# Kernel tuning notes

Hardware: AMD Instinct MI355X
Metric: run time of the kernel (lower is better)

The kernel has to match this reference:

```python
import jax, jax.numpy as jnp
import numpy as np

ATT_DIM = 512
HEADS = 8
HEAD_DIM = ATT_DIM // HEADS
D_IN = 512
LEFT_MASK = 256
RIGHT_MASK = 0
LARGE = 1e30


def pos_encoding(S, d):
    # Transformer-XL sinusoid table over relative positions S-1 .. -(S-1), length 2S-1.
    inv_freq = (1.0 / (10000.0 ** (np.arange(0, d, 2.0) / d))).astype(np.float32)
    pos = jnp.arange(S - 1, -S, -1, dtype=jnp.float32)          # [2S-1]
    ang = pos[:, None] * jnp.asarray(inv_freq)[None, :]          # [2S-1, d/2]
    # concat([sin, cos], -1) on a trailing singleton -> interleaved sin/cos per frequency
    return jnp.stack([jnp.sin(ang), jnp.cos(ang)], axis=-1).reshape(2 * S - 1, d)


def rel_shift(x):
    # x: [B, N, S, 2S-1] -> [B, N, S, S] with out[i, j] = x[i, S-1 - i + j]
    B, N, S, L = x.shape
    x = jnp.pad(x, ((0, 0), (0, 0), (0, 0), (1, 0)))             # [B,N,S,L+1]
    x = x.reshape(B, N, L + 1, S)[:, :, 1:, :]                   # [B,N,L,S]
    x = x.reshape(B, N, S, L)
    return x[:, :, :, :S]


def setup_inputs() -> dict:
    key = jax.random.key(0)
    ks = jax.random.split(key, 9)
    B, S, D = 2, 2048, D_IN
    scale = 0.02
    return {
        "x": jax.random.normal(ks[0], (B, S, D), dtype=jnp.float32),
        "Wq": jax.random.normal(ks[1], (D, ATT_DIM), dtype=jnp.float32) * scale,
        "b_con": jax.random.normal(ks[2], (ATT_DIM,), dtype=jnp.float32) * scale,
        "b_rel": jax.random.normal(ks[3], (ATT_DIM,), dtype=jnp.float32) * scale,
        "Wk": jax.random.normal(ks[4], (D, ATT_DIM), dtype=jnp.float32) * scale,
        "Wkr": jax.random.normal(ks[5], (D_IN, ATT_DIM), dtype=jnp.float32) * scale,
        "Wv": jax.random.normal(ks[6], (D, ATT_DIM), dtype=jnp.float32) * scale,
        "bv": jax.random.normal(ks[7], (ATT_DIM,), dtype=jnp.float32) * scale,
        "x_len": jax.random.randint(ks[8], (B,), 1, S + 1).astype(jnp.int32),
    }


def reference(x, Wq, b_con, b_rel, Wk, Wkr, Wv, bv, x_len):
    B, S, D = x.shape
    N, Dh = HEADS, HEAD_DIM

    # content/relative query share the kernel (TiedDense) with separate biases
    q_lin = jnp.einsum('bsd,de->bse', x, Wq)
    q_con = (q_lin + b_con).reshape(B, S, N, Dh)
    q_rel = (q_lin + b_rel).reshape(B, S, N, Dh)
    k_con = jnp.einsum('bsd,de->bse', x, Wk).reshape(B, S, N, Dh)

    content_energy = jnp.einsum('bind,bjnd->bnij', q_con, k_con)  # [B,N,S,S]

    pos_emb = pos_encoding(S, D_IN)                               # [2S-1, D]
    k_rel = (pos_emb @ Wkr).reshape(2 * S - 1, N, Dh)
    relative_energy = jnp.einsum('bind,jnd->bnij', q_rel, k_rel)  # [B,N,S,2S-1]
    relative_energy = rel_shift(relative_energy)                  # [B,N,S,S]

    energy = (content_energy + relative_energy) / jnp.sqrt(jnp.float32(Dh))

    # sequence mask over keys (broadcast [B,1,1,S]) * banded mask (band_part)
    j = jnp.arange(S)
    seq_mask = (j[None, :] < x_len[:, None]).astype(jnp.float32)[:, None, None, :]
    i = jnp.arange(S)[:, None]
    band = ((i - j[None, :] <= LEFT_MASK) & (j[None, :] - i <= RIGHT_MASK)).astype(jnp.float32)
    mask = seq_mask * band[None, None, :, :]

    masked_energy = energy - (1.0 - mask) * LARGE
    attention = jax.nn.softmax(masked_energy, axis=-1)

    v = (jnp.einsum('bsd,de->bse', x, Wv) + bv).reshape(B, S, N, Dh)
    context = jnp.einsum('bnij,bjnd->bind', attention, v).reshape(B, S, N * Dh)
    return context
```

## Files before the change

### kernel.cpp

```cpp
#include <hip/hip_runtime.h>
#include <math.h>

#define S_ 2048
#define NH 8
#define DH 64
#define CSL 320
#define LP 72

typedef __attribute__((ext_vector_type(8))) short short8;
typedef __attribute__((ext_vector_type(4))) float f32x4;
typedef unsigned short ushort_t;

__device__ __forceinline__ short bf16r(float x) {
    union { float f; unsigned u; } v; v.f = x;
    unsigned r = v.u + 0x7fffu + ((v.u >> 16) & 1u);
    return (short)(r >> 16);
}
__device__ __forceinline__ float b2f(ushort_t h) {
    union { float f; unsigned u; } v; v.u = ((unsigned)h) << 16; return v.f;
}

__global__ __launch_bounds__(256) void prep_kernel(
    const float* __restrict__ x,
    const float* __restrict__ Wq, const float* __restrict__ Wk,
    const float* __restrict__ Wv, const float* __restrict__ Wkr,
    ushort_t* __restrict__ WTq, ushort_t* __restrict__ WTk,
    ushort_t* __restrict__ WTv, ushort_t* __restrict__ WTkr,
    ushort_t* __restrict__ pos, ushort_t* __restrict__ xb16)
{
    const int widx = blockIdx.z;
    const int t = threadIdx.x;
    if (widx == 4) {
        const int base = blockIdx.y * 8 + blockIdx.x;
        const float C = -0.051905126482615036f;
        const int f = t;
#pragma unroll
        for (int rep = 0; rep < 6; ++rep) {
            const int r = base + rep * 64;
            unsigned pk = 0;
            if (r <= 256) {
                float ang = (float)r * exp2f(C * (float)f);
                unsigned s = (unsigned)(ushort_t)bf16r(sinf(ang));
                unsigned c = (unsigned)(ushort_t)bf16r(cosf(ang));
                pk = s | (c << 16);
            }
            ((unsigned*)pos)[(size_t)r * 256 + f] = pk;
        }
        return;
    }
    if (widx == 5) {
        const int sub = blockIdx.y * 8 + blockIdx.x;
        const size_t base = (size_t)sub * 32768;
#pragma unroll
        for (int it = 0; it < 8; ++it) {
            const size_t idx = base + (size_t)it * 4096 + (size_t)t * 16;
            const float* src = &x[idx];
            ushort_t t16[16];
#pragma unroll
            for (int u = 0; u < 16; ++u) t16[u] = (ushort_t)bf16r(src[u]);
            *(short8*)&xb16[idx]     = *(short8*)&t16[0];
            *(short8*)&xb16[idx + 8] = *(short8*)&t16[8];
        }
        return;
    }
    const float* W = (widx == 0) ? Wq : (widx == 1) ? Wk : (widx == 2) ? Wv : Wkr;
    ushort_t* WT   = (widx == 0) ? WTq : (widx == 1) ? WTk : (widx == 2) ? WTv : WTkr;
    const int k0 = blockIdx.x * 64, n0 = blockIdx.y * 64;
    __shared__ __align__(16) ushort_t T[64][72];
    const int srow = t >> 2, sc0 = (t & 3) * 16;
    const float* src = &W[(size_t)(k0 + srow) * 512 + n0 + sc0];
#pragma unroll
    for (int u = 0; u < 16; ++u) T[sc0 + u][srow] = (ushort_t)bf16r(src[u]);
    __syncthreads();
    ushort_t* dst = &WT[(size_t)(n0 + srow) * 512 + k0 + sc0];
    *(short8*)dst       = *(const short8*)&T[srow][sc0];
    *(short8*)(dst + 8) = *(const short8*)&T[srow][sc0 + 8];
}

__global__ __launch_bounds__(256) void qkv_gemm(
    const ushort_t* __restrict__ xb16,
    const ushort_t* __restrict__ WTq, const ushort_t* __restrict__ WTk,
    const ushort_t* __restrict__ WTv,
    const ushort_t* __restrict__ pos, const ushort_t* __restrict__ WTkr,
    const float* __restrict__ b_con, const float* __restrict__ b_rel,
    const float* __restrict__ bv, const int* __restrict__ xlen_p,
    ushort_t* __restrict__ qcon, ushort_t* __restrict__ qrel,
    ushort_t* __restrict__ kout, ushort_t* __restrict__ vT,
    ushort_t* __restrict__ krel)
{
    const int widx = blockIdx.y >> 3;
    const int tid = threadIdx.x, lane = tid & 63, w = tid >> 6;
    const int quad = lane >> 4, l16 = lane & 15;

    __shared__ __align__(16) ushort_t A_lds[128][40];
    __shared__ __align__(16) ushort_t B_lds[64][40];

    f32x4 acc[2][4];
#pragma unroll
    for (int mt = 0; mt < 2; ++mt)
#pragma unroll
        for (int nt = 0; nt < 4; ++nt) acc[mt][nt] = (f32x4){0.f, 0.f, 0.f, 0.f};

    const int arow = tid >> 1, ak0 = (tid & 1) * 16;
    const int brow = tid >> 2, bk0 = (tid & 3) * 8;

    if (widx < 2) {
        const int m0 = blockIdx.x * 128;
        {
            const int xl = xlen_p[m0 >> 11];
            const int s0 = m0 & 2047;
            if (widx == 0) { if (s0 >= xl + 256) return; }
            else           { if (s0 >= xl + 63)  return; }
        }
        const int n0 = (blockIdx.y & 7) * 64;
        const ushort_t* WT = (widx == 0) ? WTq : WTk;
        const ushort_t* xrow = &xb16[(size_t)(m0 + arow) * 512 + ak0];
        const ushort_t* wrow = &WT[(size_t)(n0 + brow) * 512 + bk0];

        short8 pa0 = *(const short8*)xrow;
        short8 pa1 = *(const short8*)(xrow + 8);
        short8 pb  = *(const short8*)wrow;

#pragma unroll 1
        for (int k0 = 0; k0 < 512; k0 += 32) {
            __syncthreads();
            *(short8*)&A_lds[arow][ak0]     = pa0;
            *(short8*)&A_lds[arow][ak0 + 8] = pa1;
            *(short8*)&B_lds[brow][bk0]     = pb;
            if (k0 < 480) {
                pa0 = *(const short8*)(xrow + k0 + 32);
                pa1 = *(const short8*)(xrow + k0 + 40);
                pb  = *(const short8*)(wrow + k0 + 32);
            }
            __syncthreads();
            short8 a0 = *(const short8*)&A_lds[w * 32 + l16][quad * 8];
            short8 a1 = *(const short8*)&A_lds[w * 32 + 16 + l16][quad * 8];
#pragma unroll
            for (int nt = 0; nt < 4; ++nt) {
                short8 bb = *(const short8*)&B_lds[nt * 16 + l16][quad * 8];
                acc[0][nt] = __builtin_amdgcn_mfma_f32_16x16x32_bf16(a0, bb, acc[0][nt], 0, 0, 0);
                acc[1][nt] = __builtin_amdgcn_mfma_f32_16x16x32_bf16(a1, bb, acc[1][nt], 0, 0, 0);
            }
        }

#pragma unroll
        for (int nt = 0; nt < 4; ++nt) {
            const int col = n0 + nt * 16 + l16;
            float bc = 0.f, br = 0.f;
            if (widx == 0) { bc = b_con[col]; br = b_rel[col]; }
#pragma unroll
            for (int mt = 0; mt < 2; ++mt) {
#pragma unroll
                for (int reg = 0; reg < 4; ++reg) {
                    const size_t m = (size_t)(m0 + w * 32 + mt * 16 + quad * 4 + reg);
                    const float val = acc[mt][nt][reg];
                    if (widx == 0) {
                        qcon[m * 512 + col] = (ushort_t)bf16r((val + bc) * 0.125f);
                        qrel[m * 512 + col] = (ushort_t)bf16r((val + br) * 0.125f);
                    } else {
                        kout[m * 512 + col] = (ushort_t)bf16r(val);
                    }
                }
            }
        }
    } else if (widx == 2) {
        const int vb = (blockIdx.y & 7) * 32 + blockIdx.x;
        const int m0d = (vb & 3) * 128;
        const int n0j = (vb >> 2) * 64;
        const ushort_t* wrow = &WTv[(size_t)(m0d + arow) * 512 + ak0];
        const ushort_t* xrow = &xb16[(size_t)(n0j + brow) * 512 + bk0];

        short8 pa0 = *(const short8*)wrow;
        short8 pa1 = *(const short8*)(wrow + 8);
        short8 pb  = *(const short8*)xrow;

#pragma unroll 1
        for (int k0 = 0; k0 < 512; k0 += 32) {
            __syncthreads();
            *(short8*)&A_lds[arow][ak0]     = pa0;
            *(short8*)&A_lds[arow][ak0 + 8] = pa1;
            *(short8*)&B_lds[brow][bk0]     = pb;
            if (k0 < 480) {
                pa0 = *(const short8*)(wrow + k0 + 32);
                pa1 = *(const short8*)(wrow + k0 + 40);
                pb  = *(const short8*)(xrow + k0 + 32);
            }
            __syncthreads();
            short8 a0 = *(const short8*)&A_lds[w * 32 + l16][quad * 8];
            short8 a1 = *(const short8*)&A_lds[w * 32 + 16 + l16][quad * 8];
#pragma unroll
            for (int nt = 0; nt < 4; ++nt) {
                short8 bb = *(const short8*)&B_lds[nt * 16 + l16][quad * 8];
                acc[0][nt] = __builtin_amdgcn_mfma_f32_16x16x32_bf16(a0, bb, acc[0][nt], 0, 0, 0);
                acc[1][nt] = __builtin_amdgcn_mfma_f32_16x16x32_bf16(a1, bb, acc[1][nt], 0, 0, 0);
            }
        }

        const int b = n0j >> 11;
#pragma unroll
        for (int mt = 0; mt < 2; ++mt) {
#pragma unroll
            for (int reg = 0; reg < 4; ++reg) {
                const int d = m0d + w * 32 + mt * 16 + quad * 4 + reg;
                const int n = d >> 6, dd = d & 63;
                const float bvv = bv[d];
#pragma unroll
                for (int nt = 0; nt < 4; ++nt) {
                    const int s = (n0j + nt * 16 + l16) & 2047;
                    vT[((size_t)((b * NH + n) * 64 + dd)) * 2048 + s] =
                        (ushort_t)bf16r(acc[mt][nt][reg] + bvv);
                }
            }
        }
    } else {
        if (blockIdx.x >= 24) return;
        const int m0 = (blockIdx.x >> 3) * 128;
        const int n0 = (blockIdx.x & 7) * 64;
        const ushort_t* prow = &pos[(size_t)(m0 + arow) * 512 + ak0];
        const ushort_t* wrow = &WTkr[(size_t)(n0 + brow) * 512 + bk0];

        short8 pa0 = *(const short8*)prow;
        short8 pa1 = *(const short8*)(prow + 8);
        short8 pb  = *(const short8*)wrow;

#pragma unroll 1
        for (int k0 = 0; k0 < 512; k0 += 32) {
            __syncthreads();
            *(short8*)&A_lds[arow][ak0]     = pa0;
            *(short8*)&A_lds[arow][ak0 + 8] = pa1;
            *(short8*)&B_lds[brow][bk0]     = pb;
            if (k0 < 480) {
                pa0 = *(const short8*)(prow + k0 + 32);
                pa1 = *(const short8*)(prow + k0 + 40);
                pb  = *(const short8*)(wrow + k0 + 32);
            }
            __syncthreads();
            short8 a0 = *(const short8*)&A_lds[w * 32 + l16][quad * 8];
            short8 a1 = *(const short8*)&A_lds[w * 32 + 16 + l16][quad * 8];
#pragma unroll
            for (int nt = 0; nt < 4; ++nt) {
                short8 bb = *(const short8*)&B_lds[nt * 16 + l16][quad * 8];
                acc[0][nt] = __builtin_amdgcn_mfma_f32_16x16x32_bf16(a0, bb, acc[0][nt], 0, 0, 0);
                acc[1][nt] = __builtin_amdgcn_mfma_f32_16x16x32_bf16(a1, bb, acc[1][nt], 0, 0, 0);
            }
        }

#pragma unroll
        for (int nt = 0; nt < 4; ++nt) {
            const int col = n0 + nt * 16 + l16;
#pragma unroll
            for (int mt = 0; mt < 2; ++mt)
#pragma unroll
                for (int reg = 0; reg < 4; ++reg) {
                    const size_t m = (size_t)(m0 + w * 32 + mt * 16 + quad * 4 + reg);
                    krel[m * 512 + col] = (ushort_t)bf16r(acc[mt][nt][reg]);
                }
        }
    }
}

__global__ __launch_bounds__(256) void rel_gemm(
    const ushort_t* __restrict__ qrel, const ushort_t* __restrict__ krel,
    const ushort_t* __restrict__ vT, const int* __restrict__ xlen_p,
    ushort_t* __restrict__ R3, float* __restrict__ vmean)
{
    const int tile = blockIdx.x, n = blockIdx.y, b = blockIdx.z;
    const int tid = threadIdx.x, lane = tid & 63, w = tid >> 6;
    const int quad = lane >> 4, l16 = lane & 15;

    __shared__ __align__(16) ushort_t A_lds[128][LP];
    __shared__ __align__(16) ushort_t B_lds[64][LP];

    if (tile == 16) {
        const int row = tid >> 2, seg = tid & 3;
        const ushort_t* src = &vT[((size_t)((b * NH + n) * 64 + row)) * 2048 + seg * 512];
        float sum = 0.f;
        for (int it = 0; it < 64; ++it) {
            short8 h = *(const short8*)(src + it * 8);
#pragma unroll
            for (int u = 0; u < 8; ++u) sum += b2f((ushort_t)h[u]);
        }
        float* scratch = (float*)A_lds;
        scratch[row * 4 + seg] = sum;
        __syncthreads();
        if (tid < 64) {
            float s = scratch[tid * 4] + scratch[tid * 4 + 1]
                    + scratch[tid * 4 + 2] + scratch[tid * 4 + 3];
            vmean[(size_t)b * 512 + n * 64 + tid] = s * (1.0f / (float)S_);
        }
        return;
    }

    const int i0 = tile * 128;
    if (i0 >= xlen_p[b] + 256) return;

    {
        const int srow = tid >> 1, sc0 = (tid & 1) * 32;
        const ushort_t* src = &qrel[((size_t)b * S_ + i0 + srow) * 512 + n * 64 + sc0];
#pragma unroll
        for (int u = 0; u < 4; ++u)
            *(short8*)&A_lds[srow][sc0 + u * 8] = *(const short8*)(src + u * 8);
    }

    const size_t rbase3 = (size_t)(b * NH + n) * S_ * CSL;
    const int srow2 = tid >> 2, sc2 = (tid & 3) * 16;

    short8 pb0, pb1;
    auto issueB = [&](int rc) {
        const ushort_t* src = &krel[(size_t)(rc * 64 + srow2) * 512 + n * 64 + sc2];
        pb0 = *(const short8*)src;
        pb1 = *(const short8*)(src + 8);
    };
    issueB(0);

#pragma unroll 1
    for (int rc = 0; rc < 5; ++rc) {
        __syncthreads();
        *(short8*)&B_lds[srow2][sc2]     = pb0;
        *(short8*)&B_lds[srow2][sc2 + 8] = pb1;
        if (rc < 4) issueB(rc + 1);
        __syncthreads();

        short8 a[2][2];
#pragma unroll
        for (int mt = 0; mt < 2; ++mt) {
            a[mt][0] = *(const short8*)&A_lds[w * 32 + mt * 16 + l16][quad * 8];
            a[mt][1] = *(const short8*)&A_lds[w * 32 + mt * 16 + l16][quad * 8 + 32];
        }
#pragma unroll
        for (int nt = 0; nt < 4; ++nt) {
            short8 b0 = *(const short8*)&B_lds[nt * 16 + l16][quad * 8];
            short8 b1 = *(const short8*)&B_lds[nt * 16 + l16][quad * 8 + 32];
            const int r = rc * 64 + nt * 16 + l16;
#pragma unroll
            for (int mt = 0; mt < 2; ++mt) {
                f32x4 s = (f32x4){0.f, 0.f, 0.f, 0.f};
                s = __builtin_amdgcn_mfma_f32_16x16x32_bf16(a[mt][0], b0, s, 0, 0, 0);
                s = __builtin_amdgcn_mfma_f32_16x16x32_bf16(a[mt][1], b1, s, 0, 0, 0);
                if (r <= 256) {
#pragma unroll
                    for (int reg = 0; reg < 4; ++reg) {
                        const int ig = i0 + w * 32 + mt * 16 + quad * 4 + reg;
                        const int cslot = (ig & 31) + 256 - r;
                        R3[rbase3 + (size_t)ig * CSL + cslot] = (ushort_t)bf16r(s[reg]);
                    }
                }
            }
        }
    }
}

__global__ __launch_bounds__(128) void attn_kernel(
    const ushort_t* __restrict__ qcon, const ushort_t* __restrict__ kbuf,
    const ushort_t* __restrict__ vT, const ushort_t* __restrict__ R3,
    const float* __restrict__ vmean, const int* __restrict__ xlen_p,
    float* __restrict__ out)
{
    const int bx = blockIdx.x;
    const int tile = ((bx & 7) << 3) | (bx >> 3);
    const int n = blockIdx.y, b = blockIdx.z;
    const int i0 = tile * 32;
    const int tid = threadIdx.x, lane = tid & 63, w = tid >> 6;
    const int quad = lane >> 4, l16 = lane & 15;
    const int xlen = xlen_p[b];

    if (i0 >= xlen + 256) {
        const int row = tid >> 2, c0 = (tid & 3) * 16;
        const float* vm = &vmean[(size_t)b * 512 + n * 64 + c0];
        float* dst = &out[((size_t)b * S_ + i0 + row) * 512 + n * 64 + c0];
#pragma unroll
        for (int u = 0; u < 16; u += 4)
            *(float4*)&dst[u] = *(const float4*)&vm[u];
        return;
    }
    int nchunk = (xlen - i0 + 256 + 63) >> 6;
    if (nchunk > 5) nchunk = 5;

    __shared__ __align__(16) ushort_t q_lds[32][LP];
    __shared__ __align__(16) ushort_t k_lds[64][LP];
    __shared__ __align__(16) ushort_t vT_lds[64][LP];
    __shared__ __align__(16) ushort_t p_lds[32][LP];
    __shared__ __align__(16) ushort_t Rl_lds[32][LP];

    {
        const int qr = tid >> 2, qc = (tid & 3) * 16;
        const ushort_t* src = &qcon[((size_t)b * S_ + i0 + qr) * 512 + n * 64 + qc];
        *(short8*)&q_lds[qr][qc]     = *(const short8*)src;
        *(short8*)&q_lds[qr][qc + 8] = *(const short8*)(src + 8);
    }

    f32x4 Oa[4];
#pragma unroll
    for (int nt = 0; nt < 4; ++nt) Oa[nt] = (f32x4){0.f, 0.f, 0.f, 0.f};
    float lpart[4] = {};

    const size_t rbase3 = (size_t)(b * NH + n) * S_ * CSL;
    const size_t vTbase = (size_t)((b * NH + n) * 64) * 2048;
    const int srow = tid >> 1, sc0 = (tid & 1) * 32;
    const int rrow = tid >> 2, rcol = (tid & 3) * 16;
    const short8 z8 = {0, 0, 0, 0, 0, 0, 0, 0};

    short8 kr[4], vr[4], kn[4], vn[4];
    short8 rcur[2], rnxt[2];

    auto issue = [&](int c, short8* kd, short8* vd, short8* rd) {
        const int jc0 = i0 - 256 + c * 64;
        const int jg = jc0 + srow;
        const bool okk = (jg >= 0);
        const ushort_t* ks = &kbuf[((size_t)b * S_ + jg) * 512 + n * 64 + sc0];
        const ushort_t* vs = &vT[vTbase + (size_t)srow * 2048 + jc0 + sc0];
#pragma unroll
        for (int u = 0; u < 4; ++u) {
            kd[u] = okk ? *(const short8*)(ks + u * 8) : z8;
            const bool okv = (jc0 + sc0 + u * 8) >= 0;
            vd[u] = okv ? *(const short8*)(vs + u * 8) : z8;
        }
        const ushort_t* Rs = &R3[rbase3 + (size_t)(i0 + rrow) * CSL + c * 64 + rcol];
        rd[0] = *(const short8*)Rs;
        rd[1] = *(const short8*)(Rs + 8);
    };

    issue(0, kr, vr, rcur);

#pragma unroll 1
    for (int c = 0; c < nchunk; ++c) {
        const int jc0 = i0 - 256 + c * 64;
        __syncthreads();
#pragma unroll
        for (int u = 0; u < 4; ++u) {
            *(short8*)&k_lds[srow][sc0 + u * 8]  = kr[u];
            *(short8*)&vT_lds[srow][sc0 + u * 8] = vr[u];
        }
        *(short8*)&Rl_lds[rrow][rcol]     = rcur[0];
        *(short8*)&Rl_lds[rrow][rcol + 8] = rcur[1];
        if (c + 1 < nchunk) issue(c + 1, kn, vn, rnxt);
        __syncthreads();

        short8 aq0 = *(const short8*)&q_lds[w * 16 + l16][quad * 8];
        short8 aq1 = *(const short8*)&q_lds[w * 16 + l16][quad * 8 + 32];
        f32x4 Sacc[4];
#pragma unroll
        for (int jt = 0; jt < 4; ++jt) {
            short8 bk0 = *(const short8*)&k_lds[jt * 16 + l16][quad * 8];
            short8 bk1 = *(const short8*)&k_lds[jt * 16 + l16][quad * 8 + 32];
            f32x4 s = (f32x4){0.f, 0.f, 0.f, 0.f};
            s = __builtin_amdgcn_mfma_f32_16x16x32_bf16(aq0, bk0, s, 0, 0, 0);
            s = __builtin_amdgcn_mfma_f32_16x16x32_bf16(aq1, bk1, s, 0, 0, 0);
            Sacc[jt] = s;
        }

#pragma unroll
        for (int jt = 0; jt < 4; ++jt) {
#pragma unroll
            for (int reg = 0; reg < 4; ++reg) {
                const int row = w * 16 + quad * 4 + reg;
                const int i = i0 + row;
                const int j = jc0 + jt * 16 + l16;
                const int r = i - j;
                const bool valid = (j >= 0) && (j < xlen) && (r >= 0) && (r <= 256);
                float rvv = b2f(Rl_lds[row][jt * 16 + l16]);
                float e = valid ? __expf(Sacc[jt][reg] + rvv) : 0.f;
                lpart[reg] += e;
                p_lds[row][jt * 16 + l16] = (ushort_t)bf16r(e);
            }
        }
        __syncthreads();

        short8 ap0 = *(const short8*)&p_lds[w * 16 + l16][quad * 8];
        short8 ap1 = *(const short8*)&p_lds[w * 16 + l16][quad * 8 + 32];
#pragma unroll
        for (int nt = 0; nt < 4; ++nt) {
            short8 bv0 = *(const short8*)&vT_lds[nt * 16 + l16][quad * 8];
            short8 bv1 = *(const short8*)&vT_lds[nt * 16 + l16][quad * 8 + 32];
            Oa[nt] = __builtin_amdgcn_mfma_f32_16x16x32_bf16(ap0, bv0, Oa[nt], 0, 0, 0);
            Oa[nt] = __builtin_amdgcn_mfma_f32_16x16x32_bf16(ap1, bv1, Oa[nt], 0, 0, 0);
        }

#pragma unroll
        for (int u = 0; u < 4; ++u) { kr[u] = kn[u]; vr[u] = vn[u]; }
        rcur[0] = rnxt[0]; rcur[1] = rnxt[1];
    }

#pragma unroll
    for (int reg = 0; reg < 4; ++reg) {
#pragma unroll
        for (int off = 1; off < 16; off <<= 1)
            lpart[reg] += __shfl_xor(lpart[reg], off, 64);
    }

#pragma unroll
    for (int reg = 0; reg < 4; ++reg) {
        const int i = i0 + w * 16 + quad * 4 + reg;
        const bool dead = (i >= xlen + 256);
        const float linv = 1.0f / lpart[reg];
#pragma unroll
        for (int nt = 0; nt < 4; ++nt) {
            const int d = n * 64 + nt * 16 + l16;
            float val = dead ? vmean[(size_t)b * 512 + d] : Oa[nt][reg] * linv;
            out[((size_t)b * S_ + i) * 512 + d] = val;
        }
    }
}

extern "C" void kernel_launch(void* const* d_in, const int* in_sizes, int n_in,
                              void* d_out, int out_size, void* d_ws, size_t ws_size,
                              hipStream_t stream) {
    const float* x     = (const float*)d_in[0];
    const float* Wq    = (const float*)d_in[1];
    const float* b_con = (const float*)d_in[2];
    const float* b_rel = (const float*)d_in[3];
    const float* Wk    = (const float*)d_in[4];
    const float* Wkr   = (const float*)d_in[5];
    const float* Wv    = (const float*)d_in[6];
    const float* bv    = (const float*)d_in[7];
    const int*   xlen  = (const int*)d_in[8];
    float* out = (float*)d_out;

    float* ws = (float*)d_ws;
    float* vmean = ws;
    ushort_t* ub   = (ushort_t*)(vmean + 1024);
    ushort_t* R3   = ub;
    ushort_t* qcon = R3   + 10485760;
    ushort_t* kbuf = qcon + 2097152;
    ushort_t* vT   = kbuf + 2097152;
    ushort_t* qrel = vT   + 2097152;
    ushort_t* xb16 = qrel + 2097152;
    ushort_t* krel = xb16 + 2097152;
    ushort_t* pos  = krel + 196608;
    ushort_t* WTq  = pos  + 196608;
    ushort_t* WTk  = WTq + 262144;
    ushort_t* WTv  = WTk + 262144;
    ushort_t* WTkr = WTv + 262144;

    prep_kernel<<<dim3(8, 8, 6), 256, 0, stream>>>(x, Wq, Wk, Wv, Wkr,
                                                   WTq, WTk, WTv, WTkr, pos, xb16);
    qkv_gemm<<<dim3(32, 25), 256, 0, stream>>>(xb16, WTq, WTk, WTv, pos, WTkr,
                                               b_con, b_rel, bv, xlen,
                                               qcon, qrel, kbuf, vT, krel);
    rel_gemm<<<dim3(17, 8, 2), 256, 0, stream>>>(qrel, krel, vT, xlen, R3, vmean);
    attn_kernel<<<dim3(64, 8, 2), 128, 0, stream>>>(qcon, kbuf, vT, R3, vmean,
                                                    xlen, out);
}
```

Measured before the change: 131.1 us.

## Fuse relative-position GEMM into attention kernel and compute V mean algebraically

Removes the separate rel_gemm kernel and its large R3 global scratch buffer. Each attention block now computes its own relative-energy band with MFMA from qrel and krel directly into a widened LDS tile, and reuses that tile for the probabilities. The V mean used for fully masked rows is computed as mean(x)·Wv + bv, using column partial sums taken in the prep kernel and a small extra block row in qkv_gemm. This cuts one launch and a large global write/read, at the cost of more LDS per attention block and extra MFMA work inside the attention kernel.

```diff
diff --git a/kernel.cpp b/kernel.cpp
--- a/kernel.cpp
+++ b/kernel.cpp
@@ -3,9 +3,8 @@
 
 #define S_ 2048
 #define NH 8
-#define DH 64
-#define CSL 320
 #define LP 72
+#define RP 328
 
 typedef __attribute__((ext_vector_type(8))) short short8;
 typedef __attribute__((ext_vector_type(4))) float f32x4;
@@ -26,7 +25,8 @@
     const float* __restrict__ Wv, const float* __restrict__ Wkr,
     ushort_t* __restrict__ WTq, ushort_t* __restrict__ WTk,
     ushort_t* __restrict__ WTv, ushort_t* __restrict__ WTkr,
-    ushort_t* __restrict__ pos, ushort_t* __restrict__ xb16)
+    ushort_t* __restrict__ pos, ushort_t* __restrict__ xb16,
+    float* __restrict__ xpart)
 {
     const int widx = blockIdx.z;
     const int t = threadIdx.x;
@@ -63,6 +63,19 @@
         }
         return;
     }
+    if (widx == 6) {
+        const int sub = blockIdx.y * 8 + blockIdx.x;
+        const int b = sub >> 5, rb = sub & 31;
+        const float* src = &x[((size_t)b * 2048 + (size_t)rb * 64) * 512];
+        float s0 = 0.f, s1 = 0.f;
+        for (int r = 0; r < 64; ++r) {
+            s0 += src[(size_t)r * 512 + t];
+            s1 += src[(size_t)r * 512 + t + 256];
+        }
+        xpart[(size_t)sub * 512 + t]       = s0;
+        xpart[(size_t)sub * 512 + t + 256] = s1;
+        return;
+    }
     const float* W = (widx == 0) ? Wq : (widx == 1) ? Wk : (widx == 2) ? Wv : Wkr;
     ushort_t* WT   = (widx == 0) ? WTq : (widx == 1) ? WTk : (widx == 2) ? WTv : WTkr;
     const int k0 = blockIdx.x * 64, n0 = blockIdx.y * 64;
@@ -84,9 +97,10 @@
     const ushort_t* __restrict__ pos, const ushort_t* __restrict__ WTkr,
     const float* __restrict__ b_con, const float* __restrict__ b_rel,
     const float* __restrict__ bv, const int* __restrict__ xlen_p,
+    const float* __restrict__ xpart,
     ushort_t* __restrict__ qcon, ushort_t* __restrict__ qrel,
     ushort_t* __restrict__ kout, ushort_t* __restrict__ vT,
-    ushort_t* __restrict__ krel)
+    ushort_t* __restrict__ krel, float* __restrict__ vmean)
 {
     const int widx = blockIdx.y >> 3;
     const int tid = threadIdx.x, lane = tid & 63, w = tid >> 6;
@@ -213,6 +227,36 @@
             }
         }
     } else {
+        if (blockIdx.y == 25) {
+            if (blockIdx.x >= 8) return;
+            float* xm = (float*)A_lds;
+            for (int idx = tid; idx < 1024; idx += 256) {
+                const int bb = idx >> 9, k = idx & 511;
+                float s = 0.f;
+                for (int p = 0; p < 32; ++p)
+                    s += xpart[(size_t)(bb * 32 + p) * 512 + k];
+                xm[bb * 512 + k] = s * (1.0f / 2048.0f);
+            }
+            __syncthreads();
+            if (tid < 64) {
+                const int d = blockIdx.x * 64 + tid;
+                const ushort_t* wrow = &WTv[(size_t)d * 512];
+                float a0 = 0.f, a1 = 0.f;
+                for (int k = 0; k < 512; k += 8) {
+                    short8 wv = *(const short8*)(wrow + k);
+#pragma unroll
+                    for (int u = 0; u < 8; ++u) {
+                        const float wf = b2f((ushort_t)wv[u]);
+                        a0 += xm[k + u] * wf;
+                        a1 += xm[512 + k + u] * wf;
+                    }
+                }
+                const float bvd = bv[d];
+                vmean[d]       = a0 + bvd;
+                vmean[512 + d] = a1 + bvd;
+            }
+            return;
+        }
         if (blockIdx.x >= 24) return;
         const int m0 = (blockIdx.x >> 3) * 128;
         const int n0 = (blockIdx.x & 7) * 64;
@@ -259,102 +303,11 @@
     }
 }
 
-__global__ __launch_bounds__(256) void rel_gemm(
-    const ushort_t* __restrict__ qrel, const ushort_t* __restrict__ krel,
-    const ushort_t* __restrict__ vT, const int* __restrict__ xlen_p,
-    ushort_t* __restrict__ R3, float* __restrict__ vmean)
-{
-    const int tile = blockIdx.x, n = blockIdx.y, b = blockIdx.z;
-    const int tid = threadIdx.x, lane = tid & 63, w = tid >> 6;
-    const int quad = lane >> 4, l16 = lane & 15;
-
-    __shared__ __align__(16) ushort_t A_lds[128][LP];
-    __shared__ __align__(16) ushort_t B_lds[64][LP];
-
-    if (tile == 16) {
-        const int row = tid >> 2, seg = tid & 3;
-        const ushort_t* src = &vT[((size_t)((b * NH + n) * 64 + row)) * 2048 + seg * 512];
-        float sum = 0.f;
-        for (int it = 0; it < 64; ++it) {
-            short8 h = *(const short8*)(src + it * 8);
-#pragma unroll
-            for (int u = 0; u < 8; ++u) sum += b2f((ushort_t)h[u]);
-        }
-        float* scratch = (float*)A_lds;
-        scratch[row * 4 + seg] = sum;
-        __syncthreads();
-        if (tid < 64) {
-            float s = scratch[tid * 4] + scratch[tid * 4 + 1]
-                    + scratch[tid * 4 + 2] + scratch[tid * 4 + 3];
-            vmean[(size_t)b * 512 + n * 64 + tid] = s * (1.0f / (float)S_);
-        }
-        return;
-    }
-
-    const int i0 = tile * 128;
-    if (i0 >= xlen_p[b] + 256) return;
-
-    {
-        const int srow = tid >> 1, sc0 = (tid & 1) * 32;
-        const ushort_t* src = &qrel[((size_t)b * S_ + i0 + srow) * 512 + n * 64 + sc0];
-#pragma unroll
-        for (int u = 0; u < 4; ++u)
-            *(short8*)&A_lds[srow][sc0 + u * 8] = *(const short8*)(src + u * 8);
-    }
-
-    const size_t rbase3 = (size_t)(b * NH + n) * S_ * CSL;
-    const int srow2 = tid >> 2, sc2 = (tid & 3) * 16;
-
-    short8 pb0, pb1;
-    auto issueB = [&](int rc) {
-        const ushort_t* src = &krel[(size_t)(rc * 64 + srow2) * 512 + n * 64 + sc2];
-        pb0 = *(const short8*)src;
-        pb1 = *(const short8*)(src + 8);
-    };
-    issueB(0);
-
-#pragma unroll 1
-    for (int rc = 0; rc < 5; ++rc) {
-        __syncthreads();
-        *(short8*)&B_lds[srow2][sc2]     = pb0;
-        *(short8*)&B_lds[srow2][sc2 + 8] = pb1;
-        if (rc < 4) issueB(rc + 1);
-        __syncthreads();
-
-        short8 a[2][2];
-#pragma unroll
-        for (int mt = 0; mt < 2; ++mt) {
-            a[mt][0] = *(const short8*)&A_lds[w * 32 + mt * 16 + l16][quad * 8];
-            a[mt][1] = *(const short8*)&A_lds[w * 32 + mt * 16 + l16][quad * 8 + 32];
-        }
-#pragma unroll
-        for (int nt = 0; nt < 4; ++nt) {
-            short8 b0 = *(const short8*)&B_lds[nt * 16 + l16][quad * 8];
-            short8 b1 = *(const short8*)&B_lds[nt * 16 + l16][quad * 8 + 32];
-            const int r = rc * 64 + nt * 16 + l16;
-#pragma unroll
-            for (int mt = 0; mt < 2; ++mt) {
-                f32x4 s = (f32x4){0.f, 0.f, 0.f, 0.f};
-                s = __builtin_amdgcn_mfma_f32_16x16x32_bf16(a[mt][0], b0, s, 0, 0, 0);
-                s = __builtin_amdgcn_mfma_f32_16x16x32_bf16(a[mt][1], b1, s, 0, 0, 0);
-                if (r <= 256) {
-#pragma unroll
-                    for (int reg = 0; reg < 4; ++reg) {
-                        const int ig = i0 + w * 32 + mt * 16 + quad * 4 + reg;
-                        const int cslot = (ig & 31) + 256 - r;
-                        R3[rbase3 + (size_t)ig * CSL + cslot] = (ushort_t)bf16r(s[reg]);
-                    }
-                }
-            }
-        }
-    }
-}
-
 __global__ __launch_bounds__(128) void attn_kernel(
-    const ushort_t* __restrict__ qcon, const ushort_t* __restrict__ kbuf,
-    const ushort_t* __restrict__ vT, const ushort_t* __restrict__ R3,
-    const float* __restrict__ vmean, const int* __restrict__ xlen_p,
-    float* __restrict__ out)
+    const ushort_t* __restrict__ qcon, const ushort_t* __restrict__ qrel,
+    const ushort_t* __restrict__ kbuf, const ushort_t* __restrict__ vT,
+    const ushort_t* __restrict__ krel, const float* __restrict__ vmean,
+    const int* __restrict__ xlen_p, float* __restrict__ out)
 {
     const int bx = blockIdx.x;
     const int tile = ((bx & 7) << 3) | (bx >> 3);
@@ -365,9 +318,9 @@
     const int xlen = xlen_p[b];
 
     if (i0 >= xlen + 256) {
-        const int row = tid >> 2, c0 = (tid & 3) * 16;
-        const float* vm = &vmean[(size_t)b * 512 + n * 64 + c0];
-        float* dst = &out[((size_t)b * S_ + i0 + row) * 512 + n * 64 + c0];
+        const int row = tid >> 2, c0f = (tid & 3) * 16;
+        const float* vm = &vmean[(size_t)b * 512 + n * 64 + c0f];
+        float* dst = &out[((size_t)b * S_ + i0 + row) * 512 + n * 64 + c0f];
 #pragma unroll
         for (int u = 0; u < 16; u += 4)
             *(float4*)&dst[u] = *(const float4*)&vm[u];
@@ -375,18 +328,46 @@
     }
     int nchunk = (xlen - i0 + 256 + 63) >> 6;
     if (nchunk > 5) nchunk = 5;
-
-    __shared__ __align__(16) ushort_t q_lds[32][LP];
+    const int c0 = (i0 < 256) ? ((256 - i0) >> 6) : 0;
+
     __shared__ __align__(16) ushort_t k_lds[64][LP];
     __shared__ __align__(16) ushort_t vT_lds[64][LP];
-    __shared__ __align__(16) ushort_t p_lds[32][LP];
-    __shared__ __align__(16) ushort_t Rl_lds[32][LP];
+    __shared__ __align__(16) ushort_t R_lds[32][RP];
+
+    const ushort_t* qc = &qcon[((size_t)b * S_ + i0 + w * 16 + l16) * 512 + n * 64 + quad * 8];
+    const short8 aq0 = *(const short8*)qc;
+    const short8 aq1 = *(const short8*)(qc + 32);
 
     {
-        const int qr = tid >> 2, qc = (tid & 3) * 16;
-        const ushort_t* src = &qcon[((size_t)b * S_ + i0 + qr) * 512 + n * 64 + qc];
-        *(short8*)&q_lds[qr][qc]     = *(const short8*)src;
-        *(short8*)&q_lds[qr][qc + 8] = *(const short8*)(src + 8);
+        const ushort_t* qr = &qrel[((size_t)b * S_ + i0 + w * 16 + l16) * 512 + n * 64 + quad * 8];
+        const short8 ar0 = *(const short8*)qr;
+        const short8 ar1 = *(const short8*)(qr + 32);
+        const ushort_t* kb = &krel[(size_t)l16 * 512 + n * 64 + quad * 8];
+        int ntmin = w + 16 - 4 * nchunk; if (ntmin < 0) ntmin = 0;
+        const int ntmax = w + 17 - 4 * c0;
+        const ushort_t* pb = kb + (size_t)ntmin * 8192;
+        short8 br0 = *(const short8*)pb;
+        short8 br1 = *(const short8*)(pb + 32);
+#pragma unroll 1
+        for (int nt = ntmin; nt < ntmax; ++nt) {
+            short8 nb0, nb1;
+            if (nt + 1 < ntmax) {
+                const ushort_t* pn = kb + (size_t)(nt + 1) * 8192;
+                nb0 = *(const short8*)pn;
+                nb1 = *(const short8*)(pn + 32);
+            }
+            f32x4 acc = (f32x4){0.f, 0.f, 0.f, 0.f};
+            acc = __builtin_amdgcn_mfma_f32_16x16x32_bf16(ar0, br0, acc, 0, 0, 0);
+            acc = __builtin_amdgcn_mfma_f32_16x16x32_bf16(ar1, br1, acc, 0, 0, 0);
+            const int r = nt * 16 + l16;
+#pragma unroll
+            for (int reg = 0; reg < 4; ++reg) {
+                const int rowq = w * 16 + quad * 4 + reg;
+                const int cs = rowq + 256 - r;
+                if (cs >= 0) R_lds[rowq][cs] = (ushort_t)bf16r(acc[reg]);
+            }
+            br0 = nb0; br1 = nb1;
+        }
     }
 
     f32x4 Oa[4];
@@ -394,16 +375,13 @@
     for (int nt = 0; nt < 4; ++nt) Oa[nt] = (f32x4){0.f, 0.f, 0.f, 0.f};
     float lpart[4] = {};
 
-    const size_t rbase3 = (size_t)(b * NH + n) * S_ * CSL;
     const size_t vTbase = (size_t)((b * NH + n) * 64) * 2048;
     const int srow = tid >> 1, sc0 = (tid & 1) * 32;
-    const int rrow = tid >> 2, rcol = (tid & 3) * 16;
     const short8 z8 = {0, 0, 0, 0, 0, 0, 0, 0};
 
     short8 kr[4], vr[4], kn[4], vn[4];
-    short8 rcur[2], rnxt[2];
-
-    auto issue = [&](int c, short8* kd, short8* vd, short8* rd) {
+
+    auto issue = [&](int c, short8* kd, short8* vd) {
         const int jc0 = i0 - 256 + c * 64;
         const int jg = jc0 + srow;
         const bool okk = (jg >= 0);
@@ -415,15 +393,12 @@
             const bool okv = (jc0 + sc0 + u * 8) >= 0;
             vd[u] = okv ? *(const short8*)(vs + u * 8) : z8;
         }
-        const ushort_t* Rs = &R3[rbase3 + (size_t)(i0 + rrow) * CSL + c * 64 + rcol];
-        rd[0] = *(const short8*)Rs;
-        rd[1] = *(const short8*)(Rs + 8);
     };
 
-    issue(0, kr, vr, rcur);
+    issue(c0, kr, vr);
 
 #pragma unroll 1
-    for (int c = 0; c < nchunk; ++c) {
+    for (int c = c0; c < nchunk; ++c) {
         const int jc0 = i0 - 256 + c * 64;
         __syncthreads();
 #pragma unroll
@@ -431,13 +406,9 @@
             *(short8*)&k_lds[srow][sc0 + u * 8]  = kr[u];
             *(short8*)&vT_lds[srow][sc0 + u * 8] = vr[u];
         }
-        *(short8*)&Rl_lds[rrow][rcol]     = rcur[0];
-        *(short8*)&Rl_lds[rrow][rcol + 8] = rcur[1];
-        if (c + 1 < nchunk) issue(c + 1, kn, vn, rnxt);
+        if (c + 1 < nchunk) issue(c + 1, kn, vn);
         __syncthreads();
 
-        short8 aq0 = *(const short8*)&q_lds[w * 16 + l16][quad * 8];
-        short8 aq1 = *(const short8*)&q_lds[w * 16 + l16][quad * 8 + 32];
         f32x4 Sacc[4];
 #pragma unroll
         for (int jt = 0; jt < 4; ++jt) {
@@ -458,16 +429,16 @@
                 const int j = jc0 + jt * 16 + l16;
                 const int r = i - j;
                 const bool valid = (j >= 0) && (j < xlen) && (r >= 0) && (r <= 256);
-                float rvv = b2f(Rl_lds[row][jt * 16 + l16]);
+                float rvv = b2f(R_lds[row][c * 64 + jt * 16 + l16]);
                 float e = valid ? __expf(Sacc[jt][reg] + rvv) : 0.f;
                 lpart[reg] += e;
-                p_lds[row][jt * 16 + l16] = (ushort_t)bf16r(e);
+                R_lds[row][c * 64 + jt * 16 + l16] = (ushort_t)bf16r(e);
             }
         }
         __syncthreads();
 
-        short8 ap0 = *(const short8*)&p_lds[w * 16 + l16][quad * 8];
-        short8 ap1 = *(const short8*)&p_lds[w * 16 + l16][quad * 8 + 32];
+        short8 ap0 = *(const short8*)&R_lds[w * 16 + l16][c * 64 + quad * 8];
+        short8 ap1 = *(const short8*)&R_lds[w * 16 + l16][c * 64 + quad * 8 + 32];
 #pragma unroll
         for (int nt = 0; nt < 4; ++nt) {
             short8 bv0 = *(const short8*)&vT_lds[nt * 16 + l16][quad * 8];
@@ -478,7 +449,6 @@
 
 #pragma unroll
         for (int u = 0; u < 4; ++u) { kr[u] = kn[u]; vr[u] = vn[u]; }
-        rcur[0] = rnxt[0]; rcur[1] = rnxt[1];
     }
 
 #pragma unroll
@@ -519,8 +489,8 @@
     float* ws = (float*)d_ws;
     float* vmean = ws;
     ushort_t* ub   = (ushort_t*)(vmean + 1024);
-    ushort_t* R3   = ub;
-    ushort_t* qcon = R3   + 10485760;
+    float* xpart   = (float*)ub;
+    ushort_t* qcon = ub   + 10485760;
     ushort_t* kbuf = qcon + 2097152;
     ushort_t* vT   = kbuf + 2097152;
     ushort_t* qrel = vT   + 2097152;
@@ -532,12 +502,12 @@
     ushort_t* WTv  = WTk + 262144;
     ushort_t* WTkr = WTv + 262144;
 
-    prep_kernel<<<dim3(8, 8, 6), 256, 0, stream>>>(x, Wq, Wk, Wv, Wkr,
-                                                   WTq, WTk, WTv, WTkr, pos, xb16);
-    qkv_gemm<<<dim3(32, 25), 256, 0, stream>>>(xb16, WTq, WTk, WTv, pos, WTkr,
-                                               b_con, b_rel, bv, xlen,
-                                               qcon, qrel, kbuf, vT, krel);
-    rel_gemm<<<dim3(17, 8, 2), 256, 0, stream>>>(qrel, krel, vT, xlen, R3, vmean);
-    attn_kernel<<<dim3(64, 8, 2), 128, 0, stream>>>(qcon, kbuf, vT, R3, vmean,
-                                                    xlen, out);
+    prep_kernel<<<dim3(8, 8, 7), 256, 0, stream>>>(x, Wq, Wk, Wv, Wkr,
+                                                   WTq, WTk, WTv, WTkr, pos, xb16,
+                                                   xpart);
+    qkv_gemm<<<dim3(32, 26), 256, 0, stream>>>(xb16, WTq, WTk, WTv, pos, WTkr,
+                                               b_con, b_rel, bv, xlen, xpart,
+                                               qcon, qrel, kbuf, vT, krel, vmean);
+    attn_kernel<<<dim3(64, 8, 2), 128, 0, stream>>>(qcon, qrel, kbuf, vT, krel,
+                                                    vmean, xlen, out);
 }
```

Measured after the change: 136.5 us. 4.1% more time.

## Enlarge attention query tile to 64 rows and skip fully-negative key chunks

Applied to the files above, without the earlier changes.

The attention kernel now processes 64 query rows per block with 256 threads instead of 32 rows with 128, so each staged K/V chunk in shared memory is reused by twice as many queries. The R3 column-slot layout in rel_gemm changes to match the 64-row tile. Query fragments are loaded straight into registers instead of through LDS, and chunks lying entirely before position zero are skipped by starting the loop at c0, which removes the j>=0 guards. This halves the grid and raises per-block LDS use, which may lower occupancy.

```diff
diff --git a/kernel.cpp b/kernel.cpp
--- a/kernel.cpp
+++ b/kernel.cpp
@@ -3,7 +3,6 @@
 
 #define S_ 2048
 #define NH 8
-#define DH 64
 #define CSL 320
 #define LP 72
 
@@ -341,7 +340,7 @@
 #pragma unroll
                     for (int reg = 0; reg < 4; ++reg) {
                         const int ig = i0 + w * 32 + mt * 16 + quad * 4 + reg;
-                        const int cslot = (ig & 31) + 256 - r;
+                        const int cslot = (ig & 63) + 256 - r;
                         R3[rbase3 + (size_t)ig * CSL + cslot] = (ushort_t)bf16r(s[reg]);
                     }
                 }
@@ -350,24 +349,24 @@
     }
 }
 
-__global__ __launch_bounds__(128) void attn_kernel(
+__global__ __launch_bounds__(256) void attn_kernel(
     const ushort_t* __restrict__ qcon, const ushort_t* __restrict__ kbuf,
     const ushort_t* __restrict__ vT, const ushort_t* __restrict__ R3,
     const float* __restrict__ vmean, const int* __restrict__ xlen_p,
     float* __restrict__ out)
 {
     const int bx = blockIdx.x;
-    const int tile = ((bx & 7) << 3) | (bx >> 3);
+    const int tile = ((bx & 7) << 2) | (bx >> 3);
     const int n = blockIdx.y, b = blockIdx.z;
-    const int i0 = tile * 32;
+    const int i0 = tile * 64;
     const int tid = threadIdx.x, lane = tid & 63, w = tid >> 6;
     const int quad = lane >> 4, l16 = lane & 15;
     const int xlen = xlen_p[b];
 
     if (i0 >= xlen + 256) {
-        const int row = tid >> 2, c0 = (tid & 3) * 16;
-        const float* vm = &vmean[(size_t)b * 512 + n * 64 + c0];
-        float* dst = &out[((size_t)b * S_ + i0 + row) * 512 + n * 64 + c0];
+        const int row = tid >> 2, cf = (tid & 3) * 16;
+        const float* vm = &vmean[(size_t)b * 512 + n * 64 + cf];
+        float* dst = &out[((size_t)b * S_ + i0 + row) * 512 + n * 64 + cf];
 #pragma unroll
         for (int u = 0; u < 16; u += 4)
             *(float4*)&dst[u] = *(const float4*)&vm[u];
@@ -375,19 +374,16 @@
     }
     int nchunk = (xlen - i0 + 256 + 63) >> 6;
     if (nchunk > 5) nchunk = 5;
-
-    __shared__ __align__(16) ushort_t q_lds[32][LP];
+    const int c0 = (i0 < 256) ? ((256 - i0) >> 6) : 0;
+
     __shared__ __align__(16) ushort_t k_lds[64][LP];
     __shared__ __align__(16) ushort_t vT_lds[64][LP];
-    __shared__ __align__(16) ushort_t p_lds[32][LP];
-    __shared__ __align__(16) ushort_t Rl_lds[32][LP];
-
-    {
-        const int qr = tid >> 2, qc = (tid & 3) * 16;
-        const ushort_t* src = &qcon[((size_t)b * S_ + i0 + qr) * 512 + n * 64 + qc];
-        *(short8*)&q_lds[qr][qc]     = *(const short8*)src;
-        *(short8*)&q_lds[qr][qc + 8] = *(const short8*)(src + 8);
-    }
+    __shared__ __align__(16) ushort_t p_lds[64][LP];
+    __shared__ __align__(16) ushort_t Rl_lds[64][LP];
+
+    const ushort_t* qc = &qcon[((size_t)b * S_ + i0 + w * 16 + l16) * 512 + n * 64 + quad * 8];
+    const short8 aq0 = *(const short8*)qc;
+    const short8 aq1 = *(const short8*)(qc + 32);
 
     f32x4 Oa[4];
 #pragma unroll
@@ -396,48 +392,38 @@
 
     const size_t rbase3 = (size_t)(b * NH + n) * S_ * CSL;
     const size_t vTbase = (size_t)((b * NH + n) * 64) * 2048;
-    const int srow = tid >> 1, sc0 = (tid & 1) * 32;
-    const int rrow = tid >> 2, rcol = (tid & 3) * 16;
-    const short8 z8 = {0, 0, 0, 0, 0, 0, 0, 0};
-
-    short8 kr[4], vr[4], kn[4], vn[4];
-    short8 rcur[2], rnxt[2];
+    const int srow = tid >> 2, sc0 = (tid & 3) * 16;
+
+    short8 kr[2], vr[2], rr[2], kn[2], vn[2], rn[2];
 
     auto issue = [&](int c, short8* kd, short8* vd, short8* rd) {
         const int jc0 = i0 - 256 + c * 64;
-        const int jg = jc0 + srow;
-        const bool okk = (jg >= 0);
-        const ushort_t* ks = &kbuf[((size_t)b * S_ + jg) * 512 + n * 64 + sc0];
+        const ushort_t* ks = &kbuf[((size_t)b * S_ + jc0 + srow) * 512 + n * 64 + sc0];
+        kd[0] = *(const short8*)ks;
+        kd[1] = *(const short8*)(ks + 8);
         const ushort_t* vs = &vT[vTbase + (size_t)srow * 2048 + jc0 + sc0];
-#pragma unroll
-        for (int u = 0; u < 4; ++u) {
-            kd[u] = okk ? *(const short8*)(ks + u * 8) : z8;
-            const bool okv = (jc0 + sc0 + u * 8) >= 0;
-            vd[u] = okv ? *(const short8*)(vs + u * 8) : z8;
-        }
-        const ushort_t* Rs = &R3[rbase3 + (size_t)(i0 + rrow) * CSL + c * 64 + rcol];
+        vd[0] = *(const short8*)vs;
+        vd[1] = *(const short8*)(vs + 8);
+        const ushort_t* Rs = &R3[rbase3 + (size_t)(i0 + srow) * CSL + c * 64 + sc0];
         rd[0] = *(const short8*)Rs;
         rd[1] = *(const short8*)(Rs + 8);
     };
 
-    issue(0, kr, vr, rcur);
+    issue(c0, kr, vr, rr);
 
 #pragma unroll 1
-    for (int c = 0; c < nchunk; ++c) {
+    for (int c = c0; c < nchunk; ++c) {
         const int jc0 = i0 - 256 + c * 64;
         __syncthreads();
-#pragma unroll
-        for (int u = 0; u < 4; ++u) {
-            *(short8*)&k_lds[srow][sc0 + u * 8]  = kr[u];
-            *(short8*)&vT_lds[srow][sc0 + u * 8] = vr[u];
-        }
-        *(short8*)&Rl_lds[rrow][rcol]     = rcur[0];
-        *(short8*)&Rl_lds[rrow][rcol + 8] = rcur[1];
-        if (c + 1 < nchunk) issue(c + 1, kn, vn, rnxt);
+        *(short8*)&k_lds[srow][sc0]      = kr[0];
+        *(short8*)&k_lds[srow][sc0 + 8]  = kr[1];
+        *(short8*)&vT_lds[srow][sc0]     = vr[0];
+        *(short8*)&vT_lds[srow][sc0 + 8] = vr[1];
+        *(short8*)&Rl_lds[srow][sc0]     = rr[0];
+        *(short8*)&Rl_lds[srow][sc0 + 8] = rr[1];
+        if (c + 1 < nchunk) issue(c + 1, kn, vn, rn);
         __syncthreads();
 
-        short8 aq0 = *(const short8*)&q_lds[w * 16 + l16][quad * 8];
-        short8 aq1 = *(const short8*)&q_lds[w * 16 + l16][quad * 8 + 32];
         f32x4 Sacc[4];
 #pragma unroll
         for (int jt = 0; jt < 4; ++jt) {
@@ -457,7 +443,7 @@
                 const int i = i0 + row;
                 const int j = jc0 + jt * 16 + l16;
                 const int r = i - j;
-                const bool valid = (j >= 0) && (j < xlen) && (r >= 0) && (r <= 256);
+                const bool valid = (j < xlen) && (r >= 0) && (r <= 256);
                 float rvv = b2f(Rl_lds[row][jt * 16 + l16]);
                 float e = valid ? __expf(Sacc[jt][reg] + rvv) : 0.f;
                 lpart[reg] += e;
@@ -476,9 +462,9 @@
             Oa[nt] = __builtin_amdgcn_mfma_f32_16x16x32_bf16(ap1, bv1, Oa[nt], 0, 0, 0);
         }
 
-#pragma unroll
-        for (int u = 0; u < 4; ++u) { kr[u] = kn[u]; vr[u] = vn[u]; }
-        rcur[0] = rnxt[0]; rcur[1] = rnxt[1];
+        kr[0] = kn[0]; kr[1] = kn[1];
+        vr[0] = vn[0]; vr[1] = vn[1];
+        rr[0] = rn[0]; rr[1] = rn[1];
     }
 
 #pragma unroll
@@ -538,6 +524,6 @@
                                                b_con, b_rel, bv, xlen,
                                                qcon, qrel, kbuf, vT, krel);
     rel_gemm<<<dim3(17, 8, 2), 256, 0, stream>>>(qrel, krel, vT, xlen, R3, vmean);
-    attn_kernel<<<dim3(64, 8, 2), 128, 0, stream>>>(qcon, kbuf, vT, R3, vmean,
+    attn_kernel<<<dim3(32, 8, 2), 256, 0, stream>>>(qcon, kbuf, vT, R3, vmean,
                                                     xlen, out);
 }
```

After: 127.9 us. -2.4%, faster.
